# Kernel optimization log

Hardware: AMD Instinct MI355X
Metric: run time of the kernel (lower is better)

Reference implementation:

```python
import jax, jax.numpy as jnp
import numpy as np

# dims matching init_kwargs
B = 4096
NFIELD = 20
NFEAT = 100000
SQL_NEMB = 16
DATA_NEMB = 16
HID = 512
K = 16          # num_experts
C = 2           # select_experts (top-k)
OUT = 1
CARD = NFIELD + NFEAT + 1  # sql embedding rows
GATE_IN = NFIELD * SQL_NEMB   # 320
EXP_IN = NFIELD * DATA_NEMB   # 320
EPS = 1e-10


def _xavier(key, shape):
    fan_in, fan_out = shape[-2], shape[-1]
    a = np.sqrt(6.0 / (fan_in + fan_out)).astype(np.float32)
    return jax.random.uniform(key, shape, jnp.float32, -a, a)


def setup_inputs() -> dict:
    key = jax.random.key(0)
    ks = jax.random.split(key, 12)
    x = jax.random.randint(ks[0], (B, NFIELD), 0, NFEAT, dtype=jnp.int64)
    sql = jax.random.randint(ks[1], (B, NFIELD), 0, CARD, dtype=jnp.int64)
    return {
        "x": x,
        "sql": sql,
        "sql_emb_w": _xavier(ks[2], (CARD, SQL_NEMB)),
        "inp_emb_w": _xavier(ks[3], (NFEAT, DATA_NEMB)),
        # gate network: Linear(GATE_IN->HID) + relu + Linear(HID->K) + softmax
        "gw1": _xavier(ks[4], (GATE_IN, HID)),
        "gb1": jnp.zeros((HID,), jnp.float32),
        "gw2": _xavier(ks[5], (HID, K)),
        "gb2": jnp.zeros((K,), jnp.float32),
        # K expert DNNs: Linear(EXP_IN->HID) + relu + Linear(HID->OUT)
        "ew1": _xavier(ks[6], (K, EXP_IN, HID)),
        "eb1": jnp.zeros((K, HID), jnp.float32),
        "ew2": _xavier(ks[7], (K, HID, OUT)),
        "eb2": jnp.zeros((K, OUT), jnp.float32),
    }


def _cv_squared(v):
    # coefficient-of-variation squared, Shazeer-style load-balancing term
    return jnp.var(v) / (jnp.mean(v) ** 2 + EPS)


def reference(x, sql, sql_emb_w, inp_emb_w, gw1, gb1, gw2, gb2, ew1, eb1, ew2, eb2):
    b = x.shape[0]
    x_emb = inp_emb_w[x].reshape(b, -1)      # [B, NFIELD*DATA_NEMB]
    sql_emb = sql_emb_w[sql].reshape(b, -1)  # [B, NFIELD*SQL_NEMB]

    # gate network -> softmax scores over K experts
    h = jax.nn.relu(sql_emb @ gw1 + gb1)
    gate_scores = jax.nn.softmax(h @ gw2 + gb2, axis=-1)  # [B, K]

    # top-C sparse gating: keep top-C scores, renormalize, zero the rest
    top_v, top_i = jax.lax.top_k(gate_scores, C)
    top_v = top_v / jnp.sum(top_v, axis=-1, keepdims=True)
    gates = jnp.zeros((b, K), gate_scores.dtype).at[jnp.arange(b)[:, None], top_i].set(top_v)

    # expert MLPs (batched over expert dim; zero gates nullify unselected experts)
    eh = jax.nn.relu(jnp.einsum('bi,kih->bkh', x_emb, ew1) + eb1)   # [B, K, HID]
    eo = jnp.einsum('bkh,kho->bko', eh, ew2) + eb2                   # [B, K, OUT]
    y = jnp.sum(gates[:, :, None] * eo, axis=1).squeeze(-1)          # [B]

    importance = jnp.sum(gates, axis=0)                              # [K]
    load = jnp.sum((gates > 0).astype(gates.dtype), axis=0)         # [K]
    loss = _cv_squared(importance) + _cv_squared(load)
    return y, loss
```

## Files before the change

kernel.cpp:

```cpp
#include <hip/hip_runtime.h>

#define Bn 4096
#define NF 20
#define NEMB 16
#define HIDN 512
#define KE 16
#define GIN 320
#define NKS 10

typedef __attribute__((ext_vector_type(8))) short short8;
typedef __attribute__((ext_vector_type(4))) float f32x4;

__device__ __forceinline__ unsigned short f2bf(float f) {
  unsigned int u = __builtin_bit_cast(unsigned int, f);
  u += 0x7fff + ((u >> 16) & 1);
  return (unsigned short)(u >> 16);
}
__device__ __forceinline__ float bf2f(unsigned short h) {
  unsigned int u = ((unsigned int)h) << 16;
  return __builtin_bit_cast(float, u);
}

__device__ __forceinline__ void gload_lds16(const unsigned short* g, void* l) {
  __builtin_amdgcn_global_load_lds(
      (const __attribute__((address_space(1))) unsigned int*)g,
      (__attribute__((address_space(3))) unsigned int*)l, 16, 0, 0);
}

__device__ __forceinline__ void vwait(int n) {
  if (n >= 5) asm volatile("s_waitcnt vmcnt(5)" ::: "memory");
  else        asm volatile("s_waitcnt vmcnt(0)" ::: "memory");
  __builtin_amdgcn_sched_barrier(0);
}

__global__ __launch_bounds__(256) void prep_kernel(
    const int* __restrict__ sql, const float* __restrict__ semb,
    const float* __restrict__ gw1, const float* __restrict__ ew1,
    unsigned short* __restrict__ SH, unsigned short* __restrict__ SL,
    unsigned short* __restrict__ GWF, unsigned short* __restrict__ EWF,
    float* __restrict__ y, int* __restrict__ cnt) {
  long long t = (long long)blockIdx.x * 256 + threadIdx.x;
  if (t < 81920) {
    int row = (int)(t / NF), f = (int)(t % NF);
    int idx = sql[row * NF + f];
    const float4* s = (const float4*)(semb + (size_t)idx * NEMB);
    float4 v[4] = {s[0], s[1], s[2], s[3]};
    const float* sf = (const float*)v;
    short8 h0, h1, l0, l1;
#pragma unroll
    for (int i = 0; i < 8; i++) {
      float a = sf[i];
      unsigned short hb = f2bf(a);
      h0[i] = (short)hb; l0[i] = (short)f2bf(a - bf2f(hb));
      a = sf[8 + i];
      hb = f2bf(a);
      h1[i] = (short)hb; l1[i] = (short)f2bf(a - bf2f(hb));
    }
    size_t o = (size_t)row * GIN + f * NEMB;
    *(short8*)(SH + o) = h0; *(short8*)(SH + o + 8) = h1;
    *(short8*)(SL + o) = l0; *(short8*)(SL + o + 8) = l1;
    return;
  }
  t -= 81920;
  if (t < 40960) {
    int s = (int)(t / 20480), r = (int)(t % 20480);
    int ks = r / 2048, r2 = r % 2048, nt = r2 / 64, l = r2 % 64;
    int k0 = ks * 32 + (l >> 4) * 8, n = nt * 16 + (l & 15);
    short8 o;
#pragma unroll
    for (int j = 0; j < 8; j++) {
      float w = gw1[(size_t)(k0 + j) * HIDN + n];
      unsigned short hb = f2bf(w);
      o[j] = (s == 0) ? (short)hb : (short)f2bf(w - bf2f(hb));
    }
    *(short8*)(GWF + ((((size_t)s * NKS + ks) * 32 + nt) * 64 + l) * 8) = o;
    return;
  }
  t -= 40960;
  if (t < 327680) {
    int e = (int)(t / 20480), r = (int)(t % 20480);
    int ks = r / 2048, r2 = r % 2048, nt = r2 / 64, l = r2 % 64;
    int k0 = ks * 32 + (l >> 4) * 8, n = nt * 16 + (l & 15);
    const float* W = ew1 + (size_t)e * GIN * HIDN;
    short8 o;
#pragma unroll
    for (int j = 0; j < 8; j++) o[j] = (short)f2bf(W[(size_t)(k0 + j) * HIDN + n]);
    *(short8*)(EWF + ((((size_t)e * NKS + ks) * 32 + nt) * 64 + l) * 8) = o;
    return;
  }
  t -= 327680;
  if (t < Bn + 1) y[t] = 0.f;
  else if (t < Bn + 1 + KE) cnt[t - (Bn + 1)] = 0;
}

__global__ __launch_bounds__(256, 2) void gate_kernel(
    const unsigned short* __restrict__ SH, const unsigned short* __restrict__ SL,
    const unsigned short* __restrict__ GWF, const float* __restrict__ gb1,
    const float* __restrict__ gw2, float* __restrict__ glp) {
  __shared__ __align__(16) unsigned short ring[3][10240];
  __shared__ float hs[64][68];
  const int tid = threadIdx.x, lane = tid & 63, wv = tid >> 6;
  const int bid = blockIdx.x;
  const int xcd = bid & 7, r_ = bid >> 3;
  const int cb = r_ & 7;
  const int band = (8 * xcd + (r_ >> 3)) * 64;
  const int ntg = cb * 4 + wv;

  short8 bh[NKS], bl[NKS];
#pragma unroll
  for (int ks = 0; ks < NKS; ks++) {
    bh[ks] = *(const short8*)(GWF + ((size_t)(ks * 32 + ntg)) * 512 + lane * 8);
    bl[ks] = *(const short8*)(GWF + ((size_t)((NKS + ks) * 32 + ntg)) * 512 + lane * 8);
  }
  const int cl = wv * 16 + (lane & 15);
  const float b1v = gb1[cb * 64 + cl];
  __builtin_amdgcn_sched_barrier(0);

#define GSTG(pi, slot)                                                        \
  {                                                                           \
    _Pragma("unroll") for (int i = 0; i < 5; i++) {                           \
      int c = wv * 5 + i;                                                     \
      int hl = c >= 10, kss = c - hl * 10;                                    \
      const unsigned short* s_ = (hl ? SL : SH) +                             \
          (size_t)(band + (pi) * 16 + (lane & 15)) * GIN + kss * 32 +         \
          (lane >> 4) * 8;                                                    \
      gload_lds16(s_, &ring[slot][c * 512 + lane * 8]);                       \
    }                                                                         \
  }

  GSTG(0, 0) GSTG(1, 1)
  __builtin_amdgcn_sched_barrier(0);

#pragma unroll
  for (int p = 0; p < 4; p++) {
    vwait(p < 3 ? 5 : 0);
    __builtin_amdgcn_s_barrier();
    __builtin_amdgcn_sched_barrier(0);
    if (p + 2 < 4) GSTG(p + 2, (p + 2) % 3)
    __builtin_amdgcn_sched_barrier(0);
    const unsigned short* rb = ring[p % 3];
    f32x4 acc = {};
#pragma unroll
    for (int ks = 0; ks < NKS; ks++) {
      short8 ah = *(const short8*)&rb[ks * 512 + lane * 8];
      short8 al = *(const short8*)&rb[(NKS + ks) * 512 + lane * 8];
      acc = __builtin_amdgcn_mfma_f32_16x16x32_bf16(ah, bh[ks], acc, 0, 0, 0);
      acc = __builtin_amdgcn_mfma_f32_16x16x32_bf16(al, bh[ks], acc, 0, 0, 0);
      acc = __builtin_amdgcn_mfma_f32_16x16x32_bf16(ah, bl[ks], acc, 0, 0, 0);
    }
#pragma unroll
    for (int j = 0; j < 4; j++)
      hs[p * 16 + (lane >> 4) * 4 + j][cl] = fmaxf(acc[j] + b1v, 0.f);
  }
  __syncthreads();

  float (*g2s)[16] = (float(*)[16])&ring[0][0];
  ((float4*)g2s)[tid] = ((const float4*)(gw2 + (size_t)cb * 64 * KE))[tid];
  __syncthreads();
#pragma unroll
  for (int it = 0; it < 4; it++) {
    int row = it * 16 + (tid >> 4), q = tid & 15;
    float s = 0.f;
#pragma unroll 8
    for (int c = 0; c < 64; c++) s = fmaf(hs[row][c], g2s[c][q], s);
    glp[((size_t)cb * Bn + band + row) * KE + q] = s;
  }
#undef GSTG
}

__global__ __launch_bounds__(256) void gate2pack_kernel(
    const float* __restrict__ glp, const float* __restrict__ gb2,
    const int* __restrict__ x, const float* __restrict__ demb,
    int* __restrict__ cnt, int* __restrict__ list, float* __restrict__ wlist,
    unsigned short* __restrict__ XEP) {
  __shared__ float part[4][64][KE];
  __shared__ int lcnt[KE];
  __shared__ int gbase[KE];
  __shared__ int selk[64][2];
  __shared__ int seli[64][2];
  const int tid = threadIdx.x;
  const int r = tid & 63, g = tid >> 6;
  const int row = blockIdx.x * 64 + r;
  if (tid < KE) lcnt[tid] = 0;
  float lg[KE];
#pragma unroll
  for (int q = 0; q < KE; q++) lg[q] = 0.f;
#pragma unroll
  for (int s2_ = 0; s2_ < 2; s2_++) {
    const float4* a = (const float4*)(glp + ((size_t)(2 * g + s2_) * Bn + row) * KE);
#pragma unroll
    for (int u = 0; u < 4; u++) {
      float4 v = a[u];
      lg[u * 4 + 0] += v.x; lg[u * 4 + 1] += v.y;
      lg[u * 4 + 2] += v.z; lg[u * 4 + 3] += v.w;
    }
  }
#pragma unroll
  for (int q = 0; q < KE; q++) part[g][r][q] = lg[q];
  __syncthreads();

  int i1 = 0, i2 = 0, o1 = 0, o2 = 0;
  float v1 = 0.f, v2 = 0.f;
  if (tid < 64) {
#pragma unroll
    for (int q = 0; q < KE; q++)
      lg[q] = part[0][tid][q] + part[1][tid][q] + part[2][tid][q] +
              part[3][tid][q] + gb2[q];
    float m = lg[0];
#pragma unroll
    for (int q = 1; q < KE; q++) m = fmaxf(m, lg[q]);
    float e[KE];
#pragma unroll
    for (int q = 0; q < KE; q++) e[q] = expf(lg[q] - m);
    v1 = e[0];
#pragma unroll
    for (int q = 1; q < KE; q++) if (e[q] > v1) { v1 = e[q]; i1 = q; }
    i2 = (i1 == 0) ? 1 : 0; v2 = e[i2];
#pragma unroll
    for (int q = 0; q < KE; q++)
      if (q != i1 && e[q] > v2) { v2 = e[q]; i2 = q; }
    o1 = atomicAdd(&lcnt[i1], 1);
    o2 = atomicAdd(&lcnt[i2], 1);
  }
  __syncthreads();
  if (tid < KE) gbase[tid] = atomicAdd(&cnt[tid], lcnt[tid]);
  __syncthreads();
  if (tid < 64) {
    int rowg = blockIdx.x * 64 + tid;
    float den = v1 + v2;
    int s1 = gbase[i1] + o1;
    list[i1 * Bn + s1] = rowg; wlist[i1 * Bn + s1] = v1 / den;
    int s2 = gbase[i2] + o2;
    list[i2 * Bn + s2] = rowg; wlist[i2 * Bn + s2] = v2 / den;
    selk[tid][0] = i1; seli[tid][0] = s1;
    selk[tid][1] = i2; seli[tid][1] = s2;
  }
  __syncthreads();

#pragma unroll 2
  for (int it = 0; it < 10; it++) {
    int t = it * 256 + tid;
    int entry = t / NF, f = t % NF;
    int rr = entry >> 1, ch = entry & 1;
    int k = selk[rr][ch], i = seli[rr][ch];
    int rid = blockIdx.x * 64 + rr;
    int idx = x[rid * NF + f];
    const float4* s = (const float4*)(demb + (size_t)idx * NEMB);
    float4 v[4] = {s[0], s[1], s[2], s[3]};
    const float* sf = (const float*)v;
    short8 q0, q1;
#pragma unroll
    for (int e = 0; e < 8; e++) {
      q0[e] = (short)f2bf(sf[e]);
      q1[e] = (short)f2bf(sf[8 + e]);
    }
    int panel = i >> 5, mt = (i >> 4) & 1, lr = i & 15;
    int ks = f >> 1, ko0 = (f & 1) * 2;
    unsigned short* d = XEP + (size_t)k * 1310720 + (size_t)panel * 10240 +
                        ks * 1024 + mt * 512 + ko0 * 128 + lr * 8;
    *(short8*)d = q0;
    *(short8*)(d + 128) = q1;
  }
}

__global__ __launch_bounds__(256, 2) void expert_kernel(
    const unsigned short* __restrict__ XEP, const unsigned short* __restrict__ EWF,
    const float* __restrict__ eb1, const float* __restrict__ ew2,
    const float* __restrict__ eb2, const int* __restrict__ cnt,
    const int* __restrict__ list, const float* __restrict__ wlist,
    float* __restrict__ y) {
  __shared__ __align__(16) unsigned short ring[3][10240];
  __shared__ float pb[16][4][32];
  const int tid = threadIdx.x, lane = tid & 63, wv = tid >> 6;
  const int bid = blockIdx.x;

  if (bid == 512) {
    float (*simp)[KE] = (float(*)[KE])&pb[0][0][0];
    float* fimp = &pb[8][0][0];
    const int kk = tid >> 4, g = tid & 15;
    const int n = cnt[kk];
    float s = 0.f;
    for (int j = g; j < n; j += 16) s += wlist[kk * Bn + j];
    simp[kk][g] = s;
    __syncthreads();
    if (tid < KE) {
      float t = 0.f;
      for (int q = 0; q < KE; q++) t += simp[tid][q];
      fimp[tid] = t;
    }
    __syncthreads();
    if (tid == 0) {
      double mi = 0.0, ml = 0.0;
      for (int q = 0; q < KE; q++) { mi += fimp[q]; ml += (double)cnt[q]; }
      mi /= KE; ml /= KE;
      double vi = 0.0, vl = 0.0;
      for (int q = 0; q < KE; q++) {
        double di = fimp[q] - mi; vi += di * di;
        double dl = (double)cnt[q] - ml; vl += dl * dl;
      }
      vi /= KE; vl /= KE;
      y[Bn] = (float)(vi / (mi * mi + 1e-10) + vl / (ml * ml + 1e-10));
    }
    return;
  }

  const int xcd = bid & 7, r_ = bid >> 3;
  const int k = xcd + 8 * (r_ & 1);
  const int cb = (r_ >> 1) & 3, qz = r_ >> 3;
  const int n = cnt[k];
  const int np = (n + 31) >> 5;
  const int npb = (np > qz) ? ((np - qz + 7) >> 3) : 0;
  if (npb == 0) return;
  const unsigned short* XEPk = XEP + (size_t)k * 1310720;
  const int kBn = k * Bn;

  float b1v[2], w2v[2];
#pragma unroll
  for (int nt = 0; nt < 2; nt++) {
    int colg = cb * 128 + (wv * 2 + nt) * 16 + (lane & 15);
    b1v[nt] = eb1[(size_t)k * HIDN + colg];
    w2v[nt] = ew2[(size_t)k * HIDN + colg];
  }
  short8 bb[2][NKS];
#pragma unroll
  for (int nt = 0; nt < 2; nt++)
#pragma unroll
    for (int ks = 0; ks < NKS; ks++)
      bb[nt][ks] = *(const short8*)(
          EWF + ((size_t)((k * NKS + ks) * 32 + cb * 8 + wv * 2 + nt)) * 512 +
          lane * 8);
  __builtin_amdgcn_sched_barrier(0);

#define ESTG(pi, slot)                                                        \
  {                                                                           \
    _Pragma("unroll") for (int i = 0; i < 5; i++) {                           \
      int c = wv * 5 + i;                                                     \
      gload_lds16(XEPk + (size_t)(pi) * 10240 + c * 512 + lane * 8,           \
                  &ring[slot][c * 512 + lane * 8]);                           \
    }                                                                         \
  }

  ESTG(qz, 0)
  if (npb > 1) ESTG(qz + 8, 1)
  __builtin_amdgcn_sched_barrier(0);

  for (int p = 0; p < npb; p++) {
    vwait((p + 1 < npb) ? 5 : 0);
    __builtin_amdgcn_s_barrier();
    __builtin_amdgcn_sched_barrier(0);
    if (p + 2 < npb) ESTG(qz + 8 * (p + 2), (p + 2) % 3)
    __builtin_amdgcn_sched_barrier(0);
    const unsigned short* rb = ring[p % 3];
    f32x4 acc[2][2] = {};
#pragma unroll
    for (int ks = 0; ks < NKS; ks++) {
      short8 a0 = *(const short8*)&rb[ks * 1024 + lane * 8];
      short8 a1 = *(const short8*)&rb[ks * 1024 + 512 + lane * 8];
      acc[0][0] = __builtin_amdgcn_mfma_f32_16x16x32_bf16(a0, bb[0][ks], acc[0][0], 0, 0, 0);
      acc[0][1] = __builtin_amdgcn_mfma_f32_16x16x32_bf16(a0, bb[1][ks], acc[0][1], 0, 0, 0);
      acc[1][0] = __builtin_amdgcn_mfma_f32_16x16x32_bf16(a1, bb[0][ks], acc[1][0], 0, 0, 0);
      acc[1][1] = __builtin_amdgcn_mfma_f32_16x16x32_bf16(a1, bb[1][ks], acc[1][1], 0, 0, 0);
    }
    float part[2][4];
#pragma unroll
    for (int mt = 0; mt < 2; mt++)
#pragma unroll
      for (int j = 0; j < 4; j++)
        part[mt][j] = fmaxf(acc[mt][0][j] + b1v[0], 0.f) * w2v[0] +
                      fmaxf(acc[mt][1][j] + b1v[1], 0.f) * w2v[1];
#pragma unroll
    for (int off = 8; off >= 1; off >>= 1)
#pragma unroll
      for (int mt = 0; mt < 2; mt++)
#pragma unroll
        for (int j = 0; j < 4; j++)
          part[mt][j] += __shfl_xor(part[mt][j], off);
    if ((lane & 15) == 0) {
#pragma unroll
      for (int mt = 0; mt < 2; mt++)
#pragma unroll
        for (int j = 0; j < 4; j++)
          pb[p][wv][mt * 16 + (lane >> 4) * 4 + j] = part[mt][j];
    }
  }
  __syncthreads();

  const float e2 = (cb == 0) ? eb2[k] : 0.f;
  for (int t = tid; t < npb * 32; t += 256) {
    int pp = t >> 5, r = t & 31;
    int i = (qz + 8 * pp) * 32 + r;
    if (i < n) {
      float v = pb[pp][0][r] + pb[pp][1][r] + pb[pp][2][r] + pb[pp][3][r];
      atomicAdd(&y[list[kBn + i]], wlist[kBn + i] * (v + e2));
    }
  }
#undef ESTG
}

extern "C" void kernel_launch(void* const* d_in, const int* in_sizes, int n_in,
                              void* d_out, int out_size, void* d_ws, size_t ws_size,
                              hipStream_t stream) {
  const int* x      = (const int*)d_in[0];
  const int* sql    = (const int*)d_in[1];
  const float* semb = (const float*)d_in[2];
  const float* demb = (const float*)d_in[3];
  const float* gw1  = (const float*)d_in[4];
  const float* gb1  = (const float*)d_in[5];
  const float* gw2  = (const float*)d_in[6];
  const float* gb2  = (const float*)d_in[7];
  const float* ew1  = (const float*)d_in[8];
  const float* eb1  = (const float*)d_in[9];
  const float* ew2  = (const float*)d_in[10];
  const float* eb2  = (const float*)d_in[11];
  float* y = (float*)d_out;

  char* ws = (char*)d_ws;
  int* cnt            = (int*)(ws);
  int* list           = (int*)(ws + 4096);
  float* wlist        = (float*)(ws + 266240);
  float* glp          = (float*)(ws + 528384);
  unsigned short* SH  = (unsigned short*)(ws + 5246976);
  unsigned short* SL  = (unsigned short*)(ws + 7868416);
  unsigned short* GWF = (unsigned short*)(ws + 10489856);
  unsigned short* EWF = (unsigned short*)(ws + 11145216);
  unsigned short* XEP = (unsigned short*)(ws + 16777216);

  prep_kernel<<<1777, 256, 0, stream>>>(sql, semb, gw1, ew1,
                                        SH, SL, GWF, EWF, y, cnt);
  gate_kernel<<<512, 256, 0, stream>>>(SH, SL, GWF, gb1, gw2, glp);
  gate2pack_kernel<<<64, 256, 0, stream>>>(glp, gb2, x, demb,
                                           cnt, list, wlist, XEP);
  expert_kernel<<<513, 256, 0, stream>>>(XEP, EWF, eb1, ew2, eb2,
                                         cnt, list, wlist, y);
}
```

Before: 63.44 us.

## Fuse gate top-k/pack stage into gate kernel via last-block-per-band counter

Removes the separate gate2pack kernel launch. The final block to finish each 64-row band, detected with an atomic counter zeroed in prep_kernel, now does the logit reduction, top-2 selection, list building and expert-input packing in-kernel. Partial logits are written and read with agent-scope relaxed atomics so the last block sees the other column blocks' results. This saves one launch and its inter-kernel gap. In exchange, the pack work now runs only in the late-finishing blocks of gate_kernel, and correctness depends on relaxed ordering plus a vmcnt wait.

```diff
diff --git a/kernel.cpp b/kernel.cpp
--- a/kernel.cpp
+++ b/kernel.cpp
@@ -33,12 +33,19 @@
   __builtin_amdgcn_sched_barrier(0);
 }
 
+__device__ __forceinline__ void st_agent(float* p, float v) {
+  __hip_atomic_store(p, v, __ATOMIC_RELAXED, __HIP_MEMORY_SCOPE_AGENT);
+}
+__device__ __forceinline__ float ld_agent(const float* p) {
+  return __hip_atomic_load(p, __ATOMIC_RELAXED, __HIP_MEMORY_SCOPE_AGENT);
+}
+
 __global__ __launch_bounds__(256) void prep_kernel(
     const int* __restrict__ sql, const float* __restrict__ semb,
     const float* __restrict__ gw1, const float* __restrict__ ew1,
     unsigned short* __restrict__ SH, unsigned short* __restrict__ SL,
     unsigned short* __restrict__ GWF, unsigned short* __restrict__ EWF,
-    float* __restrict__ y, int* __restrict__ cnt) {
+    float* __restrict__ y, int* __restrict__ cnt, int* __restrict__ done) {
   long long t = (long long)blockIdx.x * 256 + threadIdx.x;
   if (t < 81920) {
     int row = (int)(t / NF), f = (int)(t % NF);
@@ -91,19 +98,26 @@
   t -= 327680;
   if (t < Bn + 1) y[t] = 0.f;
   else if (t < Bn + 1 + KE) cnt[t - (Bn + 1)] = 0;
+  else if (t < Bn + 1 + KE + 64) done[t - (Bn + 1 + KE)] = 0;
 }
 
 __global__ __launch_bounds__(256, 2) void gate_kernel(
     const unsigned short* __restrict__ SH, const unsigned short* __restrict__ SL,
     const unsigned short* __restrict__ GWF, const float* __restrict__ gb1,
-    const float* __restrict__ gw2, float* __restrict__ glp) {
+    const float* __restrict__ gw2, const float* __restrict__ gb2,
+    const int* __restrict__ x, const float* __restrict__ demb,
+    float* __restrict__ glp, int* __restrict__ done, int* __restrict__ cnt,
+    int* __restrict__ list, float* __restrict__ wlist,
+    unsigned short* __restrict__ XEP) {
   __shared__ __align__(16) unsigned short ring[3][10240];
   __shared__ float hs[64][68];
+  __shared__ int sOld;
   const int tid = threadIdx.x, lane = tid & 63, wv = tid >> 6;
   const int bid = blockIdx.x;
   const int xcd = bid & 7, r_ = bid >> 3;
   const int cb = r_ & 7;
-  const int band = (8 * xcd + (r_ >> 3)) * 64;
+  const int bandIdx = 8 * xcd + (r_ >> 3);
+  const int band = bandIdx * 64;
   const int ntg = cb * 4 + wv;
 
   short8 bh[NKS], bl[NKS];
@@ -163,40 +177,36 @@
     float s = 0.f;
 #pragma unroll 8
     for (int c = 0; c < 64; c++) s = fmaf(hs[row][c], g2s[c][q], s);
-    glp[((size_t)cb * Bn + band + row) * KE + q] = s;
+    st_agent(&glp[((size_t)cb * Bn + band + row) * KE + q], s);
   }
 #undef GSTG
-}
-
-__global__ __launch_bounds__(256) void gate2pack_kernel(
-    const float* __restrict__ glp, const float* __restrict__ gb2,
-    const int* __restrict__ x, const float* __restrict__ demb,
-    int* __restrict__ cnt, int* __restrict__ list, float* __restrict__ wlist,
-    unsigned short* __restrict__ XEP) {
-  __shared__ float part[4][64][KE];
-  __shared__ int lcnt[KE];
-  __shared__ int gbase[KE];
-  __shared__ int selk[64][2];
-  __shared__ int seli[64][2];
-  const int tid = threadIdx.x;
-  const int r = tid & 63, g = tid >> 6;
-  const int row = blockIdx.x * 64 + r;
+
+  asm volatile("s_waitcnt vmcnt(0)" ::: "memory");
+  __syncthreads();
+  if (tid == 0) sOld = atomicAdd(&done[bandIdx], 1);
+  __syncthreads();
+  if (sOld != 7) return;
+
+  int* lcnt = (int*)&ring[0][0];
+  int* gbase = lcnt + KE;
+  int (*selk)[2] = (int(*)[2])(gbase + KE);
+  int (*seli)[2] = (int(*)[2])(selk + 64);
+  float (*part)[64][KE] = (float(*)[64][KE])&hs[0][0];
+
   if (tid < KE) lcnt[tid] = 0;
+  const int r2 = tid & 63, g2 = tid >> 6;
+  const int row2 = band + r2;
   float lg[KE];
 #pragma unroll
   for (int q = 0; q < KE; q++) lg[q] = 0.f;
 #pragma unroll
-  for (int s2_ = 0; s2_ < 2; s2_++) {
-    const float4* a = (const float4*)(glp + ((size_t)(2 * g + s2_) * Bn + row) * KE);
-#pragma unroll
-    for (int u = 0; u < 4; u++) {
-      float4 v = a[u];
-      lg[u * 4 + 0] += v.x; lg[u * 4 + 1] += v.y;
-      lg[u * 4 + 2] += v.z; lg[u * 4 + 3] += v.w;
-    }
-  }
-#pragma unroll
-  for (int q = 0; q < KE; q++) part[g][r][q] = lg[q];
+  for (int sl2 = 0; sl2 < 2; sl2++) {
+    const float* a = glp + ((size_t)(2 * g2 + sl2) * Bn + row2) * KE;
+#pragma unroll
+    for (int q = 0; q < KE; q++) lg[q] += ld_agent(a + q);
+  }
+#pragma unroll
+  for (int q = 0; q < KE; q++) part[g2][r2][q] = lg[q];
   __syncthreads();
 
   int i1 = 0, i2 = 0, o1 = 0, o2 = 0;
@@ -226,7 +236,7 @@
   if (tid < KE) gbase[tid] = atomicAdd(&cnt[tid], lcnt[tid]);
   __syncthreads();
   if (tid < 64) {
-    int rowg = blockIdx.x * 64 + tid;
+    int rowg = band + tid;
     float den = v1 + v2;
     int s1 = gbase[i1] + o1;
     list[i1 * Bn + s1] = rowg; wlist[i1 * Bn + s1] = v1 / den;
@@ -243,7 +253,7 @@
     int entry = t / NF, f = t % NF;
     int rr = entry >> 1, ch = entry & 1;
     int k = selk[rr][ch], i = seli[rr][ch];
-    int rid = blockIdx.x * 64 + rr;
+    int rid = band + rr;
     int idx = x[rid * NF + f];
     const float4* s = (const float4*)(demb + (size_t)idx * NEMB);
     float4 v[4] = {s[0], s[1], s[2], s[3]};
@@ -416,6 +426,7 @@
 
   char* ws = (char*)d_ws;
   int* cnt            = (int*)(ws);
+  int* done           = (int*)(ws + 2048);
   int* list           = (int*)(ws + 4096);
   float* wlist        = (float*)(ws + 266240);
   float* glp          = (float*)(ws + 528384);
@@ -426,10 +437,9 @@
   unsigned short* XEP = (unsigned short*)(ws + 16777216);
 
   prep_kernel<<<1777, 256, 0, stream>>>(sql, semb, gw1, ew1,
-                                        SH, SL, GWF, EWF, y, cnt);
-  gate_kernel<<<512, 256, 0, stream>>>(SH, SL, GWF, gb1, gw2, glp);
-  gate2pack_kernel<<<64, 256, 0, stream>>>(glp, gb2, x, demb,
-                                           cnt, list, wlist, XEP);
+                                        SH, SL, GWF, EWF, y, cnt, done);
+  gate_kernel<<<512, 256, 0, stream>>>(SH, SL, GWF, gb1, gw2, gb2, x, demb,
+                                       glp, done, cnt, list, wlist, XEP);
   expert_kernel<<<513, 256, 0, stream>>>(XEP, EWF, eb1, ew2, eb2,
                                          cnt, list, wlist, y);
 }
```

Measured after the change: 75.93 us. +19.7%, slower.
